# Kernel optimization log

Measured on AMD Instinct MI355X. Metric: run time of the kernel, lower is better.

The kernel has to match this reference:

```python
import jax, jax.numpy as jnp
import numpy as np

N = 100000       # nodes
E = 1600000      # edges (before self-loops)
IN = 32          # input_dim
HID = 64         # hidden_dim
HEADS = 4
HO = HID // HEADS  # per-head out of gat1
OUT = 32         # output_dim
HID2 = HID // 2
BN_EPS = 1e-5
NEG_SLOPE = 0.2  # PyG GATConv default leaky relu slope


def setup_inputs() -> dict:
    key = jax.random.key(0)
    ks = jax.random.split(key, 28)
    f32 = jnp.float32
    rn = lambda k, s, sc=0.1: jax.random.normal(k, s, f32) * sc
    inp = {}
    inp["x"] = jax.random.normal(ks[0], (N, IN), f32)
    inp["edge_index"] = jax.random.randint(ks[1], (2, E), 0, N, jnp.int32)
    # GATConv 1: in=IN, heads=HEADS, out/head=HO, concat
    inp["W1"] = rn(ks[2], (IN, HEADS * HO))
    inp["att_src1"] = rn(ks[3], (HEADS, HO))
    inp["att_dst1"] = rn(ks[4], (HEADS, HO))
    inp["b1"] = rn(ks[5], (HEADS * HO,))
    # GATConv 2: in=HID, heads=1, out=OUT, no concat (mean)
    inp["W2"] = rn(ks[6], (HID, OUT))
    inp["att_src2"] = rn(ks[7], (1, OUT))
    inp["att_dst2"] = rn(ks[8], (1, OUT))
    inp["b2"] = rn(ks[9], (OUT,))
    # BatchNorms (inference mode: running stats)
    inp["bn1_g"] = jnp.ones((HID,), f32)
    inp["bn1_b"] = jnp.zeros((HID,), f32)
    inp["bn1_m"] = rn(ks[10], (HID,), 0.1)
    inp["bn1_v"] = jax.random.uniform(ks[11], (HID,), f32, 0.5, 1.5)
    inp["bn2_g"] = jnp.ones((OUT,), f32)
    inp["bn2_b"] = jnp.zeros((OUT,), f32)
    inp["bn2_m"] = rn(ks[12], (OUT,), 0.1)
    inp["bn2_v"] = jax.random.uniform(ks[13], (OUT,), f32, 0.5, 1.5)
    # classifier: OUT -> HID2 -> 3
    inp["cls_w1"] = rn(ks[14], (OUT, HID2))
    inp["cls_b1"] = rn(ks[15], (HID2,))
    inp["cls_w2"] = rn(ks[16], (HID2, 3))
    inp["cls_b2"] = rn(ks[17], (3,))
    inp["reg_w1"] = rn(ks[18], (OUT, HID2))
    inp["reg_b1"] = rn(ks[19], (HID2,))
    inp["reg_w2"] = rn(ks[20], (HID2, 1))
    inp["reg_b2"] = rn(ks[21], (1,))
    return inp


def _segment_softmax(e, seg, n):
    # e: [E, H]; softmax over edges sharing the same destination segment
    m = jax.ops.segment_max(e, seg, num_segments=n)
    ex = jnp.exp(e - m[seg])
    s = jax.ops.segment_sum(ex, seg, num_segments=n)
    return ex / (s[seg] + 1e-16)


def _gat(x, src, dst, W, a_src, a_dst, b, heads, ho, concat):
    n = x.shape[0]
    h = (x @ W).reshape(n, heads, ho)                    # [N,H,F]
    e = (h * a_src).sum(-1)[src] + (h * a_dst).sum(-1)[dst]  # [E,H]
    e = jax.nn.leaky_relu(e, NEG_SLOPE)
    alpha = _segment_softmax(e, dst, n)                  # [E,H]
    out = jax.ops.segment_sum(h[src] * alpha[:, :, None], dst, num_segments=n)
    out = out.reshape(n, heads * ho) if concat else out.mean(axis=1)
    return out + b


def _bn(x, g, b, m, v):
    return (x - m) * jax.lax.rsqrt(v + BN_EPS) * g + b


def reference(x, edge_index, W1, att_src1, att_dst1, b1, W2, att_src2, att_dst2, b2,
              bn1_g, bn1_b, bn1_m, bn1_v, bn2_g, bn2_b, bn2_m, bn2_v,
              cls_w1, cls_b1, cls_w2, cls_b2, reg_w1, reg_b1, reg_w2, reg_b2):
    n = x.shape[0]
    # PyG GATConv default add_self_loops=True
    loops = jnp.arange(n, dtype=edge_index.dtype)
    src = jnp.concatenate([edge_index[0], loops])
    dst = jnp.concatenate([edge_index[1], loops])

    h = _gat(x, src, dst, W1, att_src1, att_dst1, b1, HEADS, HO, True)   # [N, HID]
    h = jax.nn.relu(_bn(h, bn1_g, bn1_b, bn1_m, bn1_v))
    emb = _gat(h, src, dst, W2, att_src2, att_dst2, b2, 1, OUT, False)   # [N, OUT]
    emb = jax.nn.relu(_bn(emb, bn2_g, bn2_b, bn2_m, bn2_v))

    roles = jax.nn.relu(emb @ cls_w1 + cls_b1) @ cls_w2 + cls_b2          # [N, 3]
    energy = jax.nn.relu(emb @ reg_w1 + reg_b1) @ reg_w2 + reg_b2         # [N, 1]
    return emb, roles, energy
```

## Files before the change

kernel.cpp:

```cpp
#include <hip/hip_runtime.h>
#include <hip/hip_bf16.h>

#define NN 100000
#define EE 1600000
#define ETOT (EE + NN)
#define IND 32
#define HIDD 64
#define NHEADS 4
#define OUTD 32
#define HID2D 32

#define BSH 8
#define NBUCK 391
#define CAP 5120
#define EPB 2048

typedef unsigned int uint;

__device__ __forceinline__ uint pack2(float a, float b) {
  uint lo = (uint)__bfloat16_as_ushort(__float2bfloat16(a));
  uint hi = (uint)__bfloat16_as_ushort(__float2bfloat16(b));
  return (hi << 16) | lo;
}
__device__ __forceinline__ float lo2f(uint w) { return __uint_as_float(w << 16); }
__device__ __forceinline__ float hi2f(uint w) { return __uint_as_float(w & 0xFFFF0000u); }

__global__ __launch_bounds__(256) void k_lin1(
    const float* __restrict__ x, const float* __restrict__ W1,
    const float* __restrict__ atsrc, const float* __restrict__ atdst,
    uint* __restrict__ h1u, float* __restrict__ as1, float* __restrict__ ad1) {
  __shared__ float Ws[IND * HIDD];
  __shared__ float xs[8 * IND];
  __shared__ float atS[HIDD], atD[HIDD];
  int t = threadIdx.x;
  for (int i = t; i < IND * HIDD; i += 256) Ws[i] = W1[i];
  if (t < HIDD) { atS[t] = atsrc[t]; atD[t] = atdst[t]; }
  xs[t] = x[blockIdx.x * 256 + t];
  __syncthreads();
  int nl = t >> 5, tl = t & 31;
  int node = blockIdx.x * 8 + nl;
  int j0 = 2 * tl, j1 = j0 + 1;
  float a0 = 0.f, a1 = 0.f;
#pragma unroll
  for (int k = 0; k < IND; k++) {
    float xv = xs[nl * IND + k];
    a0 += xv * Ws[k * HIDD + j0];
    a1 += xv * Ws[k * HIDD + j1];
  }
  h1u[node * 32 + tl] = pack2(a0, a1);
  float ps = a0 * atS[j0] + a1 * atS[j1];
  float pd = a0 * atD[j0] + a1 * atD[j1];
#pragma unroll
  for (int off = 4; off >= 1; off >>= 1) {
    ps += __shfl_down(ps, off, 8);
    pd += __shfl_down(pd, off, 8);
  }
  if ((tl & 7) == 0) {
    as1[node * NHEADS + (tl >> 3)] = ps;
    ad1[node * NHEADS + (tl >> 3)] = pd;
  }
}

__global__ __launch_bounds__(256) void k_lin2(
    const float* __restrict__ hbn, const float* __restrict__ W2,
    const float* __restrict__ atsrc, const float* __restrict__ atdst,
    uint* __restrict__ h2u, float* __restrict__ as2, float* __restrict__ ad2) {
  __shared__ float Ws[HIDD * OUTD];
  __shared__ float xs[16 * HIDD];
  __shared__ float atS[OUTD], atD[OUTD];
  int t = threadIdx.x;
  for (int i = t; i < HIDD * OUTD; i += 256) Ws[i] = W2[i];
  if (t < OUTD) { atS[t] = atsrc[t]; atD[t] = atdst[t]; }
  for (int i = t; i < 16 * HIDD; i += 256) xs[i] = hbn[blockIdx.x * 16 * HIDD + i];
  __syncthreads();
  int nl = t >> 4, tl = t & 15;
  int node = blockIdx.x * 16 + nl;
  int j0 = 2 * tl, j1 = j0 + 1;
  float a0 = 0.f, a1 = 0.f;
#pragma unroll
  for (int k = 0; k < HIDD; k++) {
    float xv = xs[nl * HIDD + k];
    a0 += xv * Ws[k * OUTD + j0];
    a1 += xv * Ws[k * OUTD + j1];
  }
  h2u[node * 16 + tl] = pack2(a0, a1);
  float ps = a0 * atS[j0] + a1 * atS[j1];
  float pd = a0 * atD[j0] + a1 * atD[j1];
#pragma unroll
  for (int off = 8; off >= 1; off >>= 1) {
    ps += __shfl_down(ps, off, 16);
    pd += __shfl_down(pd, off, 16);
  }
  if (tl == 0) { as2[node] = ps; ad2[node] = pd; }
}

__global__ __launch_bounds__(256) void k_bin(const int* __restrict__ ei,
                                             int* __restrict__ bcur,
                                             int* __restrict__ bins) {
  __shared__ int cnt[NBUCK];
  int t = threadIdx.x;
  for (int i = t; i < NBUCK; i += 256) cnt[i] = 0;
  __syncthreads();
  int base = blockIdx.x * EPB;
  int recs[8], bks[8];
#pragma unroll
  for (int k = 0; k < 8; k++) {
    int i = base + k * 256 + t;
    recs[k] = -1; bks[k] = 0;
    if (i < ETOT) {
      int s, d;
      if (i < EE) { s = ei[i]; d = ei[EE + i]; } else { s = i - EE; d = s; }
      recs[k] = (s << BSH) | (d & ((1 << BSH) - 1));
      bks[k] = d >> BSH;
      atomicAdd(&cnt[bks[k]], 1);
    }
  }
  __syncthreads();
  for (int i = t; i < NBUCK; i += 256) cnt[i] = atomicAdd(&bcur[i], cnt[i]);
  __syncthreads();
#pragma unroll
  for (int k = 0; k < 8; k++) {
    if (recs[k] >= 0) {
      int pos = atomicAdd(&cnt[bks[k]], 1);
      bins[bks[k] * CAP + pos] = recs[k];
    }
  }
}

__global__ __launch_bounds__(256) void k_csr(const int* __restrict__ bcur,
                                             const int* __restrict__ bins,
                                             int* __restrict__ rowp,
                                             int* __restrict__ srcs) {
  __shared__ int lrec[CAP];
  __shared__ int sA[512], sB[512];
  __shared__ int ldeg[256];
  int b = blockIdx.x, t = threadIdx.x;
  sA[t] = (t < NBUCK) ? bcur[t] : 0;
  sA[t + 256] = (t + 256 < NBUCK) ? bcur[t + 256] : 0;
  __syncthreads();
  int* in = sA; int* out = sB;
  for (int off = 1; off < 512; off <<= 1) {
    for (int i = t; i < 512; i += 256)
      out[i] = in[i] + ((i >= off) ? in[i - off] : 0);
    __syncthreads();
    int* tmp = in; in = out; out = tmp;
  }
  int gb = (b == 0) ? 0 : in[b - 1];
  if (b == 0 && t == 0) rowp[NN] = ETOT;
  __syncthreads();
  int count = bcur[b]; if (count > CAP) count = CAP;
  ldeg[t] = 0;
  __syncthreads();
  for (int i = t; i < count; i += 256) {
    int r = bins[b * CAP + i];
    lrec[i] = r;
    atomicAdd(&ldeg[r & 255], 1);
  }
  __syncthreads();
  int dv = ldeg[t];
  sA[t] = dv;
  __syncthreads();
  in = sA; out = sB;
  for (int off = 1; off < 256; off <<= 1) {
    out[t] = in[t] + ((t >= off) ? in[t - off] : 0);
    __syncthreads();
    int* tmp = in; in = out; out = tmp;
  }
  int nb = b << BSH;
  int ex = in[t] - dv;
  if (nb + t < NN) rowp[nb + t] = gb + ex;
  ldeg[t] = ex;
  __syncthreads();
  for (int i = t; i < count; i += 256) {
    int r = lrec[i];
    int pos = atomicAdd(&ldeg[r & 255], 1);
    srcs[gb + pos] = r >> BSH;
  }
}

__global__ __launch_bounds__(256) void k_agg1(
    const int* __restrict__ rowp, const int* __restrict__ srcs,
    const uint* __restrict__ h1u, const float* __restrict__ as1,
    const float* __restrict__ ad1, const float* __restrict__ b1,
    const float* __restrict__ g, const float* __restrict__ bb,
    const float* __restrict__ m, const float* __restrict__ v,
    float* __restrict__ hbn) {
  int t = threadIdx.x;
  int wid = t >> 6, lane = t & 63;
  int nA = blockIdx.x * 8 + wid * 2;
  int nB = nA + 1;
  int slot = lane >> 3;
  int fl = lane & 7;
  int hd = fl >> 1;
  int stA = rowp[nA], eA = rowp[nA + 1], eB = rowp[nB + 1];
  int stB = eA;
  int lpA = eA - 1, lpB = eB - 1;
  float advA = ad1[nA * NHEADS + hd];
  float advB = ad1[nB * NHEADS + hd];
  const uint4* h14 = (const uint4*)h1u;
  float accA[8] = {0,0,0,0,0,0,0,0}, accB[8] = {0,0,0,0,0,0,0,0};
  float lA = 0.f, lB = 0.f;
  int pA = stA + slot, pB = stB + slot;
  int sA0 = srcs[pA < lpA ? pA : lpA];
  int sB0 = srcs[pB < lpB ? pB : lpB];
  uint4 wA = h14[sA0 * 8 + fl];
  uint4 wB = h14[sB0 * 8 + fl];
  float asA = as1[sA0 * NHEADS + hd];
  float asB = as1[sB0 * NHEADS + hd];
  int p1A = pA + 8, p1B = pB + 8;
  int sA1 = srcs[p1A < lpA ? p1A : lpA];
  int sB1 = srcs[p1B < lpB ? p1B : lpB];
  while (pA < eA || pB < eB) {
    uint4 wnA = h14[sA1 * 8 + fl];
    uint4 wnB = h14[sB1 * 8 + fl];
    float anA = as1[sA1 * NHEADS + hd];
    float anB = as1[sB1 * NHEADS + hd];
    int p2A = p1A + 8, p2B = p1B + 8;
    int sA2 = srcs[p2A < lpA ? p2A : lpA];
    int sB2 = srcs[p2B < lpB ? p2B : lpB];
    if (pA < eA) {
      float e = asA + advA;
      e = fmaxf(e, 0.2f * e);
      float ex = __expf(e);
      lA += ex;
      accA[0] += ex * lo2f(wA.x); accA[1] += ex * hi2f(wA.x);
      accA[2] += ex * lo2f(wA.y); accA[3] += ex * hi2f(wA.y);
      accA[4] += ex * lo2f(wA.z); accA[5] += ex * hi2f(wA.z);
      accA[6] += ex * lo2f(wA.w); accA[7] += ex * hi2f(wA.w);
    }
    if (pB < eB) {
      float e = asB + advB;
      e = fmaxf(e, 0.2f * e);
      float ex = __expf(e);
      lB += ex;
      accB[0] += ex * lo2f(wB.x); accB[1] += ex * hi2f(wB.x);
      accB[2] += ex * lo2f(wB.y); accB[3] += ex * hi2f(wB.y);
      accB[4] += ex * lo2f(wB.z); accB[5] += ex * hi2f(wB.z);
      accB[6] += ex * lo2f(wB.w); accB[7] += ex * hi2f(wB.w);
    }
    wA = wnA; wB = wnB; asA = anA; asB = anB;
    sA1 = sA2; sB1 = sB2;
    pA = p1A; pB = p1B; p1A = p2A; p1B = p2B;
  }
#pragma unroll
  for (int off = 8; off <= 32; off <<= 1) {
#pragma unroll
    for (int i = 0; i < 8; i++) {
      accA[i] += __shfl_xor(accA[i], off, 64);
      accB[i] += __shfl_xor(accB[i], off, 64);
    }
    lA += __shfl_xor(lA, off, 64);
    lB += __shfl_xor(lB, off, 64);
  }
  if (slot < 2) {
    int node = slot == 0 ? nA : nB;
    float lsum = slot == 0 ? lA : lB;
    float li = 1.f / (lsum + 1e-16f);
    int fb = fl * 8;
    float o[8];
#pragma unroll
    for (int i = 0; i < 8; i++) {
      int j = fb + i;
      float av = slot == 0 ? accA[i] : accB[i];
      float ov = av * li + b1[j];
      ov = (ov - m[j]) * rsqrtf(v[j] + 1e-5f) * g[j] + bb[j];
      o[i] = fmaxf(ov, 0.f);
    }
    float4* dst = (float4*)(hbn + node * HIDD + fb);
    dst[0] = make_float4(o[0], o[1], o[2], o[3]);
    dst[1] = make_float4(o[4], o[5], o[6], o[7]);
  }
}

__global__ __launch_bounds__(256) void k_agg2(
    const int* __restrict__ rowp, const int* __restrict__ srcs,
    const uint* __restrict__ h2u, const float* __restrict__ as2,
    const float* __restrict__ ad2, const float* __restrict__ b2v,
    const float* __restrict__ g, const float* __restrict__ bb,
    const float* __restrict__ m, const float* __restrict__ v,
    float* __restrict__ out_emb) {
  int t = threadIdx.x;
  int wid = t >> 6, lane = t & 63;
  int nA = blockIdx.x * 8 + wid * 2;
  int nB = nA + 1;
  int slot = lane >> 3;
  int fl = lane & 7;
  int stA = rowp[nA], eA = rowp[nA + 1], eB = rowp[nB + 1];
  int stB = eA;
  int lpA = eA - 1, lpB = eB - 1;
  float advA = ad2[nA], advB = ad2[nB];
  const uint2* h22 = (const uint2*)h2u;
  float accA[4] = {0,0,0,0}, accB[4] = {0,0,0,0};
  float lA = 0.f, lB = 0.f;
  int pA = stA + slot, pB = stB + slot;
  int sA0 = srcs[pA < lpA ? pA : lpA];
  int sB0 = srcs[pB < lpB ? pB : lpB];
  uint2 wA = h22[sA0 * 8 + fl];
  uint2 wB = h22[sB0 * 8 + fl];
  float asA = as2[sA0], asB = as2[sB0];
  int p1A = pA + 8, p1B = pB + 8;
  int sA1 = srcs[p1A < lpA ? p1A : lpA];
  int sB1 = srcs[p1B < lpB ? p1B : lpB];
  while (pA < eA || pB < eB) {
    uint2 wnA = h22[sA1 * 8 + fl];
    uint2 wnB = h22[sB1 * 8 + fl];
    float anA = as2[sA1], anB = as2[sB1];
    int p2A = p1A + 8, p2B = p1B + 8;
    int sA2 = srcs[p2A < lpA ? p2A : lpA];
    int sB2 = srcs[p2B < lpB ? p2B : lpB];
    if (pA < eA) {
      float e = asA + advA;
      e = fmaxf(e, 0.2f * e);
      float ex = __expf(e);
      lA += ex;
      accA[0] += ex * lo2f(wA.x); accA[1] += ex * hi2f(wA.x);
      accA[2] += ex * lo2f(wA.y); accA[3] += ex * hi2f(wA.y);
    }
    if (pB < eB) {
      float e = asB + advB;
      e = fmaxf(e, 0.2f * e);
      float ex = __expf(e);
      lB += ex;
      accB[0] += ex * lo2f(wB.x); accB[1] += ex * hi2f(wB.x);
      accB[2] += ex * lo2f(wB.y); accB[3] += ex * hi2f(wB.y);
    }
    wA = wnA; wB = wnB; asA = anA; asB = anB;
    sA1 = sA2; sB1 = sB2;
    pA = p1A; pB = p1B; p1A = p2A; p1B = p2B;
  }
#pragma unroll
  for (int off = 8; off <= 32; off <<= 1) {
#pragma unroll
    for (int i = 0; i < 4; i++) {
      accA[i] += __shfl_xor(accA[i], off, 64);
      accB[i] += __shfl_xor(accB[i], off, 64);
    }
    lA += __shfl_xor(lA, off, 64);
    lB += __shfl_xor(lB, off, 64);
  }
  if (slot < 2) {
    int node = slot == 0 ? nA : nB;
    float lsum = slot == 0 ? lA : lB;
    float li = 1.f / (lsum + 1e-16f);
    int fb = fl * 4;
    float o[4];
#pragma unroll
    for (int i = 0; i < 4; i++) {
      int j = fb + i;
      float av = slot == 0 ? accA[i] : accB[i];
      float ov = av * li + b2v[j];
      ov = (ov - m[j]) * rsqrtf(v[j] + 1e-5f) * g[j] + bb[j];
      o[i] = fmaxf(ov, 0.f);
    }
    *(float4*)(out_emb + node * OUTD + fb) = make_float4(o[0], o[1], o[2], o[3]);
  }
}

__global__ __launch_bounds__(256) void k_mlp(
    const float* __restrict__ embf,
    const float* __restrict__ cw1, const float* __restrict__ cb1,
    const float* __restrict__ cw2, const float* __restrict__ cb2,
    const float* __restrict__ rw1, const float* __restrict__ rb1,
    const float* __restrict__ rw2, const float* __restrict__ rb2,
    float* __restrict__ out_roles, float* __restrict__ out_energy) {
  __shared__ float C1[OUTD * HID2D], R1[OUTD * HID2D];
  __shared__ float C2[HID2D * 3], CB1[HID2D], RB1[HID2D], R2[HID2D];
  __shared__ float CB2v[3], RB2v;
  int t = threadIdx.x;
  for (int i = t; i < OUTD * HID2D; i += 256) { C1[i] = cw1[i]; R1[i] = rw1[i]; }
  if (t < HID2D) { CB1[t] = cb1[t]; RB1[t] = rb1[t]; R2[t] = rw2[t]; }
  if (t < HID2D * 3) C2[t] = cw2[t];
  if (t < 3) CB2v[t] = cb2[t];
  if (t == 0) RB2v = rb2[0];
  __syncthreads();
  int node = blockIdx.x * 256 + t;
  if (node >= NN) return;
  float e[OUTD];
#pragma unroll
  for (int k = 0; k < OUTD; k++) e[k] = embf[node * OUTD + k];
  float r0 = CB2v[0], r1 = CB2v[1], r2 = CB2v[2], en = RB2v;
  for (int j = 0; j < HID2D; j++) {
    float hc = CB1[j], hr = RB1[j];
#pragma unroll
    for (int k = 0; k < OUTD; k++) {
      hc += e[k] * C1[k * HID2D + j];
      hr += e[k] * R1[k * HID2D + j];
    }
    hc = fmaxf(hc, 0.f);
    hr = fmaxf(hr, 0.f);
    r0 += hc * C2[j * 3 + 0];
    r1 += hc * C2[j * 3 + 1];
    r2 += hc * C2[j * 3 + 2];
    en += hr * R2[j];
  }
  out_roles[node * 3 + 0] = r0;
  out_roles[node * 3 + 1] = r1;
  out_roles[node * 3 + 2] = r2;
  out_energy[node] = en;
}

extern "C" void kernel_launch(void* const* d_in, const int* in_sizes, int n_in,
                              void* d_out, int out_size, void* d_ws, size_t ws_size,
                              hipStream_t stream) {
  const float* x    = (const float*)d_in[0];
  const int*   ei   = (const int*)d_in[1];
  const float* W1   = (const float*)d_in[2];
  const float* as1w = (const float*)d_in[3];
  const float* ad1w = (const float*)d_in[4];
  const float* b1   = (const float*)d_in[5];
  const float* W2   = (const float*)d_in[6];
  const float* as2w = (const float*)d_in[7];
  const float* ad2w = (const float*)d_in[8];
  const float* b2v  = (const float*)d_in[9];
  const float* bn1g = (const float*)d_in[10];
  const float* bn1b = (const float*)d_in[11];
  const float* bn1m = (const float*)d_in[12];
  const float* bn1v = (const float*)d_in[13];
  const float* bn2g = (const float*)d_in[14];
  const float* bn2b = (const float*)d_in[15];
  const float* bn2m = (const float*)d_in[16];
  const float* bn2v = (const float*)d_in[17];
  const float* cw1  = (const float*)d_in[18];
  const float* cb1  = (const float*)d_in[19];
  const float* cw2  = (const float*)d_in[20];
  const float* cb2  = (const float*)d_in[21];
  const float* rw1  = (const float*)d_in[22];
  const float* rb1  = (const float*)d_in[23];
  const float* rw2  = (const float*)d_in[24];
  const float* rb2  = (const float*)d_in[25];

  uint*  h1u = (uint*)d_ws;
  float* hbn = (float*)(h1u + NN * 32);
  float* as1 = hbn + NN * HIDD;
  float* ad1 = as1 + NN * NHEADS;
  int* rowp  = (int*)(ad1 + NN * NHEADS);
  int* srcs  = rowp + NN + 1;
  int* bcur  = srcs + ETOT;
  int* bins  = bcur + 512;
  uint* h2u  = h1u;
  float* as2 = as1;
  float* ad2 = ad1;

  float* out        = (float*)d_out;
  float* out_emb    = out;
  float* out_roles  = out + NN * OUTD;
  float* out_energy = out + NN * (OUTD + 3);

  hipMemsetAsync(bcur, 0, 512 * sizeof(int), stream);
  k_bin<<<(ETOT + EPB - 1) / EPB, 256, 0, stream>>>(ei, bcur, bins);
  k_csr<<<NBUCK, 256, 0, stream>>>(bcur, bins, rowp, srcs);
  k_lin1<<<NN / 8, 256, 0, stream>>>(x, W1, as1w, ad1w, h1u, as1, ad1);
  k_agg1<<<NN / 8, 256, 0, stream>>>(rowp, srcs, h1u, as1, ad1, b1, bn1g, bn1b, bn1m, bn1v, hbn);
  k_lin2<<<NN / 16, 256, 0, stream>>>(hbn, W2, as2w, ad2w, h2u, as2, ad2);
  k_agg2<<<NN / 8, 256, 0, stream>>>(rowp, srcs, h2u, as2, ad2, b2v, bn2g, bn2b, bn2m, bn2v, out_emb);
  k_mlp<<<(NN + 255) / 256, 256, 0, stream>>>(out_emb, cw1, cb1, cw2, cb2, rw1, rb1, rw2, rb2, out_roles, out_energy);
}
```

Before: 326.8 us.

## Fuse edge binning with first linear layer and pre-scale CSR source indices

```diff
diff --git a/kernel.cpp b/kernel.cpp
--- a/kernel.cpp
+++ b/kernel.cpp
@@ -14,6 +14,8 @@
 #define NBUCK 391
 #define CAP 5120
 #define EPB 2048
+#define NBBIN ((ETOT + EPB - 1) / EPB)
+#define NBLIN1 (NN / 8)
 
 typedef unsigned int uint;
 
@@ -25,39 +27,71 @@
 __device__ __forceinline__ float lo2f(uint w) { return __uint_as_float(w << 16); }
 __device__ __forceinline__ float hi2f(uint w) { return __uint_as_float(w & 0xFFFF0000u); }
 
-__global__ __launch_bounds__(256) void k_lin1(
+__global__ __launch_bounds__(256) void k_pre(
+    const int* __restrict__ ei, int* __restrict__ bcur, int* __restrict__ bins,
     const float* __restrict__ x, const float* __restrict__ W1,
     const float* __restrict__ atsrc, const float* __restrict__ atdst,
     uint* __restrict__ h1u, float* __restrict__ as1, float* __restrict__ ad1) {
+  __shared__ int cnt[NBUCK];
   __shared__ float Ws[IND * HIDD];
   __shared__ float xs[8 * IND];
   __shared__ float atS[HIDD], atD[HIDD];
   int t = threadIdx.x;
-  for (int i = t; i < IND * HIDD; i += 256) Ws[i] = W1[i];
-  if (t < HIDD) { atS[t] = atsrc[t]; atD[t] = atdst[t]; }
-  xs[t] = x[blockIdx.x * 256 + t];
-  __syncthreads();
-  int nl = t >> 5, tl = t & 31;
-  int node = blockIdx.x * 8 + nl;
-  int j0 = 2 * tl, j1 = j0 + 1;
-  float a0 = 0.f, a1 = 0.f;
-#pragma unroll
-  for (int k = 0; k < IND; k++) {
-    float xv = xs[nl * IND + k];
-    a0 += xv * Ws[k * HIDD + j0];
-    a1 += xv * Ws[k * HIDD + j1];
-  }
-  h1u[node * 32 + tl] = pack2(a0, a1);
-  float ps = a0 * atS[j0] + a1 * atS[j1];
-  float pd = a0 * atD[j0] + a1 * atD[j1];
-#pragma unroll
-  for (int off = 4; off >= 1; off >>= 1) {
-    ps += __shfl_down(ps, off, 8);
-    pd += __shfl_down(pd, off, 8);
-  }
-  if ((tl & 7) == 0) {
-    as1[node * NHEADS + (tl >> 3)] = ps;
-    ad1[node * NHEADS + (tl >> 3)] = pd;
+  if (blockIdx.x < NBBIN) {
+    for (int i = t; i < NBUCK; i += 256) cnt[i] = 0;
+    __syncthreads();
+    int base = blockIdx.x * EPB;
+    int recs[8], bks[8];
+#pragma unroll
+    for (int k = 0; k < 8; k++) {
+      int i = base + k * 256 + t;
+      recs[k] = -1; bks[k] = 0;
+      if (i < ETOT) {
+        int s, d;
+        if (i < EE) { s = ei[i]; d = ei[EE + i]; } else { s = i - EE; d = s; }
+        recs[k] = (s << BSH) | (d & ((1 << BSH) - 1));
+        bks[k] = d >> BSH;
+        atomicAdd(&cnt[bks[k]], 1);
+      }
+    }
+    __syncthreads();
+    for (int i = t; i < NBUCK; i += 256) cnt[i] = atomicAdd(&bcur[i], cnt[i]);
+    __syncthreads();
+#pragma unroll
+    for (int k = 0; k < 8; k++) {
+      if (recs[k] >= 0) {
+        int pos = atomicAdd(&cnt[bks[k]], 1);
+        bins[bks[k] * CAP + pos] = recs[k];
+      }
+    }
+  } else {
+    int bid = blockIdx.x - NBBIN;
+    for (int i = t; i < IND * HIDD; i += 256) Ws[i] = W1[i];
+    if (t < HIDD) { atS[t] = atsrc[t]; atD[t] = atdst[t]; }
+    xs[t] = x[bid * 256 + t];
+    __syncthreads();
+    int nl = t >> 5, tl = t & 31;
+    int node = bid * 8 + nl;
+    int j0 = 2 * tl, j1 = j0 + 1;
+    float a0 = 0.f, a1 = 0.f;
+#pragma unroll
+    for (int k = 0; k < IND; k++) {
+      float xv = xs[nl * IND + k];
+      a0 += xv * Ws[k * HIDD + j0];
+      a1 += xv * Ws[k * HIDD + j1];
+    }
+    h1u[node * 32 + tl] = pack2(a0, a1);
+    float ps = a0 * atS[j0] + a1 * atS[j1];
+    float pd = a0 * atD[j0] + a1 * atD[j1];
+#pragma unroll
+    for (int off = 4; off >= 1; off >>= 1) {
+      ps += __shfl_down(ps, off, 8);
+      pd += __shfl_down(pd, off, 8);
+    }
+    if ((tl & 7) == 0) {
+      as1[node * NHEADS + (tl >> 3)] = ps;
+      ad1[node * NHEADS + (tl >> 3)] = pd;
+    }
   }
 }
 
@@ -94,39 +128,6 @@
   if (tl == 0) { as2[node] = ps; ad2[node] = pd; }
 }
 
-__global__ __launch_bounds__(256) void k_bin(const int* __restrict__ ei,
-                                             int* __restrict__ bcur,
-                                             int* __restrict__ bins) {
-  __shared__ int cnt[NBUCK];
-  int t = threadIdx.x;
-  for (int i = t; i < NBUCK; i += 256) cnt[i] = 0;
-  __syncthreads();
-  int base = blockIdx.x * EPB;
-  int recs[8], bks[8];
-#pragma unroll
-  for (int k = 0; k < 8; k++) {
-    int i = base + k * 256 + t;
-    recs[k] = -1; bks[k] = 0;
-    if (i < ETOT) {
-      int s, d;
-      if (i < EE) { s = ei[i]; d = ei[EE + i]; } else { s = i - EE; d = s; }
-      recs[k] = (s << BSH) | (d & ((1 << BSH) - 1));
-      bks[k] = d >> BSH;
-      atomicAdd(&cnt[bks[k]], 1);
-    }
-  }
-  __syncthreads();
-  for (int i = t; i < NBUCK; i += 256) cnt[i] = atomicAdd(&bcur[i], cnt[i]);
-  __syncthreads();
-#pragma unroll
-  for (int k = 0; k < 8; k++) {
-    if (recs[k] >= 0) {
-      int pos = atomicAdd(&cnt[bks[k]], 1);
-      bins[bks[k] * CAP + pos] = recs[k];
-    }
-  }
-}
-
 __global__ __launch_bounds__(256) void k_csr(const int* __restrict__ bcur,
                                              const int* __restrict__ bins,
                                              int* __restrict__ rowp,
@@ -135,6 +136,10 @@
   __shared__ int sA[512], sB[512];
   __shared__ int ldeg[256];
   int b = blockIdx.x, t = threadIdx.x;
+  if (b == 0) {
+    if (t < 64) srcs[ETOT + t] = 0;
+    if (t == 0) rowp[NN] = ETOT;
+  }
   sA[t] = (t < NBUCK) ? bcur[t] : 0;
   sA[t + 256] = (t + 256 < NBUCK) ? bcur[t + 256] : 0;
   __syncthreads();
@@ -146,7 +151,6 @@
     int* tmp = in; in = out; out = tmp;
   }
   int gb = (b == 0) ? 0 : in[b - 1];
-  if (b == 0 && t == 0) rowp[NN] = ETOT;
   __syncthreads();
   int count = bcur[b]; if (count > CAP) count = CAP;
   ldeg[t] = 0;
@@ -174,11 +178,11 @@
   for (int i = t; i < count; i += 256) {
     int r = lrec[i];
     int pos = atomicAdd(&ldeg[r & 255], 1);
-    srcs[gb + pos] = r >> BSH;
-  }
-}
-
-__global__ __launch_bounds__(256) void k_agg1(
+    srcs[gb + pos] = (r >> BSH) << 3;
+  }
+}
+
+__global__ __launch_bounds__(256, 4) void k_agg1(
     const int* __restrict__ rowp, const int* __restrict__ srcs,
     const uint* __restrict__ h1u, const float* __restrict__ as1,
     const float* __restrict__ ad1, const float* __restrict__ b1,
@@ -194,30 +198,29 @@
   int hd = fl >> 1;
   int stA = rowp[nA], eA = rowp[nA + 1], eB = rowp[nB + 1];
   int stB = eA;
-  int lpA = eA - 1, lpB = eB - 1;
   float advA = ad1[nA * NHEADS + hd];
   float advB = ad1[nB * NHEADS + hd];
   const uint4* h14 = (const uint4*)h1u;
   float accA[8] = {0,0,0,0,0,0,0,0}, accB[8] = {0,0,0,0,0,0,0,0};
   float lA = 0.f, lB = 0.f;
   int pA = stA + slot, pB = stB + slot;
-  int sA0 = srcs[pA < lpA ? pA : lpA];
-  int sB0 = srcs[pB < lpB ? pB : lpB];
-  uint4 wA = h14[sA0 * 8 + fl];
-  uint4 wB = h14[sB0 * 8 + fl];
-  float asA = as1[sA0 * NHEADS + hd];
-  float asB = as1[sB0 * NHEADS + hd];
+  int sA0 = srcs[pA];
+  int sB0 = srcs[pB];
+  uint4 wA = h14[sA0 + fl];
+  uint4 wB = h14[sB0 + fl];
+  float asA = as1[(sA0 >> 1) + hd];
+  float asB = as1[(sB0 >> 1) + hd];
   int p1A = pA + 8, p1B = pB + 8;
-  int sA1 = srcs[p1A < lpA ? p1A : lpA];
-  int sB1 = srcs[p1B < lpB ? p1B : lpB];
+  int sA1 = srcs[p1A];
+  int sB1 = srcs[p1B];
   while (pA < eA || pB < eB) {
-    uint4 wnA = h14[sA1 * 8 + fl];
-    uint4 wnB = h14[sB1 * 8 + fl];
-    float anA = as1[sA1 * NHEADS + hd];
-    float anB = as1[sB1 * NHEADS + hd];
+    uint4 wnA = h14[sA1 + fl];
+    uint4 wnB = h14[sB1 + fl];
+    float anA = as1[(sA1 >> 1) + hd];
+    float anB = as1[(sB1 >> 1) + hd];
     int p2A = p1A + 8, p2B = p1B + 8;
-    int sA2 = srcs[p2A < lpA ? p2A : lpA];
-    int sB2 = srcs[p2B < lpB ? p2B : lpB];
+    int sA2 = srcs[p2A < ETOT ? p2A : ETOT];
+    int sB2 = srcs[p2B < ETOT ? p2B : ETOT];
     if (pA < eA) {
       float e = asA + advA;
       e = fmaxf(e, 0.2f * e);
@@ -272,7 +275,7 @@
   }
 }
 
-__global__ __launch_bounds__(256) void k_agg2(
+__global__ __launch_bounds__(256, 4) void k_agg2(
     const int* __restrict__ rowp, const int* __restrict__ srcs,
     const uint* __restrict__ h2u, const float* __restrict__ as2,
     const float* __restrict__ ad2, const float* __restrict__ b2v,
@@ -287,27 +290,26 @@
   int fl = lane & 7;
   int stA = rowp[nA], eA = rowp[nA + 1], eB = rowp[nB + 1];
   int stB = eA;
-  int lpA = eA - 1, lpB = eB - 1;
   float advA = ad2[nA], advB = ad2[nB];
   const uint2* h22 = (const uint2*)h2u;
   float accA[4] = {0,0,0,0}, accB[4] = {0,0,0,0};
   float lA = 0.f, lB = 0.f;
   int pA = stA + slot, pB = stB + slot;
-  int sA0 = srcs[pA < lpA ? pA : lpA];
-  int sB0 = srcs[pB < lpB ? pB : lpB];
-  uint2 wA = h22[sA0 * 8 + fl];
-  uint2 wB = h22[sB0 * 8 + fl];
-  float asA = as2[sA0], asB = as2[sB0];
+  int sA0 = srcs[pA];
+  int sB0 = srcs[pB];
+  uint2 wA = h22[sA0 + fl];
+  uint2 wB = h22[sB0 + fl];
+  float asA = as2[sA0 >> 3], asB = as2[sB0 >> 3];
   int p1A = pA + 8, p1B = pB + 8;
-  int sA1 = srcs[p1A < lpA ? p1A : lpA];
-  int sB1 = srcs[p1B < lpB ? p1B : lpB];
+  int sA1 = srcs[p1A];
+  int sB1 = srcs[p1B];
   while (pA < eA || pB < eB) {
-    uint2 wnA = h22[sA1 * 8 + fl];
-    uint2 wnB = h22[sB1 * 8 + fl];
-    float anA = as2[sA1], anB = as2[sB1];
+    uint2 wnA = h22[sA1 + fl];
+    uint2 wnB = h22[sB1 + fl];
+    float anA = as2[sA1 >> 3], anB = as2[sB1 >> 3];
     int p2A = p1A + 8, p2B = p1B + 8;
-    int sA2 = srcs[p2A < lpA ? p2A : lpA];
-    int sB2 = srcs[p2B < lpB ? p2B : lpB];
+    int sA2 = srcs[p2A < ETOT ? p2A : ETOT];
+    int sB2 = srcs[p2B < ETOT ? p2B : ETOT];
     if (pA < eA) {
       float e = asA + advA;
       e = fmaxf(e, 0.2f * e);
@@ -435,7 +437,7 @@
   float* ad1 = as1 + NN * NHEADS;
   int* rowp  = (int*)(ad1 + NN * NHEADS);
   int* srcs  = rowp + NN + 1;
-  int* bcur  = srcs + ETOT;
+  int* bcur  = srcs + ETOT + 64;
   int* bins  = bcur + 512;
   uint* h2u  = h1u;
   float* as2 = as1;
@@ -447,9 +449,8 @@
   float* out_energy = out + NN * (OUTD + 3);
 
   hipMemsetAsync(bcur, 0, 512 * sizeof(int), stream);
-  k_bin<<<(ETOT + EPB - 1) / EPB, 256, 0, stream>>>(ei, bcur, bins);
+  k_pre<<<NBBIN + NBLIN1, 256, 0, stream>>>(ei, bcur, bins, x, W1, as1w, ad1w, h1u, as1, ad1);
   k_csr<<<NBUCK, 256, 0, stream>>>(bcur, bins, rowp, srcs);
-  k_lin1<<<NN / 8, 256, 0, stream>>>(x, W1, as1w, ad1w, h1u, as1, ad1);
   k_agg1<<<NN / 8, 256, 0, stream>>>(rowp, srcs, h1u, as1, ad1, b1, bn1g, bn1b, bn1m, bn1v, hbn);
   k_lin2<<<NN / 16, 256, 0, stream>>>(hbn, W2, as2w, ad2w, h2u, as2, ad2);
   k_agg2<<<NN / 8, 256, 0, stream>>>(rowp, srcs, h2u, as2, ad2, b2v, bn2g, bn2b, bn2m, bn2v, out_emb);
```

Result: no change. 330.5 us (+1.1%).
